# Kernel optimization log

Measured on AMD Instinct MI355X. Metric: run time of the kernel, lower is better.

The kernel has to match this reference:

```python
import jax, jax.numpy as jnp
import numpy as np
from jax import lax

HEADS, DIM = 8, 8
T = HEADS * DIM            # total_dim = 64
C_IN, C_OUT = 256, 256
B, H, W = 8, 128, 128
BN_EPS = 1e-5


def setup_inputs() -> dict:
    key = jax.random.key(0)
    ks = jax.random.split(key, 9)
    return {
        "x": jax.random.normal(ks[0], (B, C_IN, H, W), jnp.float32),
        "W_qkv": jax.random.normal(ks[1], (3 * T, C_IN), jnp.float32) * 0.05,
        "W_p": jax.random.normal(ks[2], (3 * HEADS, DIM, DIM), jnp.float32) * 0.1,
        "W_d": jax.random.normal(ks[3], (3 * T, 1, 3, 3), jnp.float32) * 0.1,
        "W_ffn": jax.random.normal(ks[4], (C_OUT, 2 * T), jnp.float32) * 0.1,
        "bn_gamma": jax.random.uniform(ks[5], (C_OUT,), jnp.float32, 0.5, 1.5),
        "bn_beta": jax.random.normal(ks[6], (C_OUT,), jnp.float32) * 0.1,
        "bn_mean": jax.random.normal(ks[7], (C_OUT,), jnp.float32) * 0.1,
        "bn_var": jax.random.uniform(ks[8], (C_OUT,), jnp.float32, 0.5, 1.5),
    }


def reference(x, W_qkv, W_p, W_d, W_ffn, bn_gamma, bn_beta, bn_mean, bn_var):
    b, _, h, w = x.shape
    # qkv: 1x1 conv, no bias -> (B, 3T, H, W)
    qkv = jnp.einsum('bchw,oc->bohw', x, W_qkv)
    # p_conv: grouped 1x1 conv, groups = 3*heads, group size = dim
    p = qkv.reshape(b, 3 * HEADS, DIM, h, w)
    p = jnp.einsum('bgihw,goi->bgohw', p, W_p).reshape(b, 3 * T, h, w)
    # d_conv: depthwise 3x3 conv, padding 1
    d = lax.conv_general_dilated(
        p, W_d, window_strides=(1, 1), padding='SAME',
        dimension_numbers=('NCHW', 'OIHW', 'NCHW'), feature_group_count=3 * T)
    # multi-scale concat -> (B, 6T, H, W) -> (B, 2*heads, 3*dim, HW) -> (B, 2*heads, HW, 3*dim)
    g = jnp.concatenate([qkv, d], axis=1)
    g = g.reshape(b, 2 * HEADS, 3 * DIM, h * w).transpose(0, 1, 3, 2)
    q = jax.nn.relu(g[..., :DIM])
    k = jax.nn.relu(g[..., DIM:2 * DIM])
    v = g[..., 2 * DIM:]
    # padding trick: append a column of ones to v for normalization
    v1 = jnp.concatenate([v, jnp.ones(v.shape[:-1] + (1,), v.dtype)], axis=-1)
    kv = jnp.einsum('bgnd,bgne->bgde', k, v1)     # (B, 2h, dim, dim+1)
    o = jnp.einsum('bgnd,bgde->bgne', q, kv)      # (B, 2h, HW, dim+1)
    o = o[..., :DIM] / (o[..., DIM:] + 1e-15)
    o = o.transpose(0, 1, 3, 2).reshape(b, 2 * T, h, w)
    # ffn: 1x1 conv + BatchNorm (eval mode, running stats)
    y = jnp.einsum('bchw,oc->bohw', o, W_ffn)
    scale = bn_gamma / jnp.sqrt(bn_var + BN_EPS)
    return y * scale[:, None, None] + (bn_beta - bn_mean * scale)[:, None, None]
```

## Files before the change

kernel.cpp:

```cpp
#include <hip/hip_runtime.h>

#define NB    8
#define NCIN  256
#define NH    128
#define NW    128
#define NHW   16384
#define NQKV  192
#define NCOUT 256

#define K1_BK  16
#define K1_LDB 132
#define K1_LDA 64

__global__ __launch_bounds__(256) void k1_qkv(
    const float* __restrict__ x, const float* __restrict__ Wq,
    float* __restrict__ qkv)
{
  __shared__ float Bs[2][K1_BK][K1_LDB];
  __shared__ float As[2][K1_BK][K1_LDA];

  const int tid = threadIdx.x;
  const int b   = blockIdx.x >> 7;
  const int n0  = (blockIdx.x & 127) << 7;
  const int m0  = blockIdx.y << 6;

  const int bk = tid >> 4;
  const int bn = (tid & 15) << 3;
  const int am = tid >> 2;
  const int ak = (tid & 3) << 2;
  const float* bP = x + (size_t)b * NCIN * NHW + (size_t)bk * NHW + n0 + bn;
  const float* aP = Wq + ((size_t)(m0 + am) << 8) + ak;

  const int tx = tid & 31;
  const int ty = tid >> 5;

  float4 rb0, rb1, ra;
  rb0 = *(const float4*)(bP);
  rb1 = *(const float4*)(bP + 4);
  ra  = *(const float4*)(aP);

  *(float4*)&Bs[0][bk][bn]     = rb0;
  *(float4*)&Bs[0][bk][bn + 4] = rb1;
  As[0][ak + 0][am] = ra.x;
  As[0][ak + 1][am] = ra.y;
  As[0][ak + 2][am] = ra.z;
  As[0][ak + 3][am] = ra.w;
  __syncthreads();

  float acc[8][4];
#pragma unroll
  for (int i = 0; i < 8; ++i)
#pragma unroll
    for (int j = 0; j < 4; ++j) acc[i][j] = 0.f;

  int cur = 0;
  for (int t = 0; t < 16; ++t) {
    if (t < 15) {
      const float* bq = bP + (size_t)(t + 1) * K1_BK * NHW;
      rb0 = *(const float4*)(bq);
      rb1 = *(const float4*)(bq + 4);
      ra  = *(const float4*)(aP + (t + 1) * K1_BK);
    }

#pragma unroll
    for (int kk = 0; kk < K1_BK; ++kk) {
      const float4 a0 = *(const float4*)&As[cur][kk][ty * 4];
      const float4 a1 = *(const float4*)&As[cur][kk][32 + ty * 4];
      const float4 bv = *(const float4*)&Bs[cur][kk][tx * 4];
      const float a[8]  = {a0.x, a0.y, a0.z, a0.w, a1.x, a1.y, a1.z, a1.w};
      const float bb[4] = {bv.x, bv.y, bv.z, bv.w};
#pragma unroll
      for (int i = 0; i < 8; ++i)
#pragma unroll
        for (int j = 0; j < 4; ++j) acc[i][j] = fmaf(a[i], bb[j], acc[i][j]);
    }

    if (t < 15) {
      const int nxt = cur ^ 1;
      *(float4*)&Bs[nxt][bk][bn]     = rb0;
      *(float4*)&Bs[nxt][bk][bn + 4] = rb1;
      As[nxt][ak + 0][am] = ra.x;
      As[nxt][ak + 1][am] = ra.y;
      As[nxt][ak + 2][am] = ra.z;
      As[nxt][ak + 3][am] = ra.w;
      __syncthreads();
      cur = nxt;
    }
  }

  float* outB = qkv + (size_t)b * NQKV * NHW + n0 + tx * 4;
#pragma unroll
  for (int i = 0; i < 8; ++i) {
    const int m = m0 + ((i < 4) ? (ty * 4 + i) : (32 + ty * 4 + (i - 4)));
    float4 v = {acc[i][0], acc[i][1], acc[i][2], acc[i][3]};
    *(float4*)(outB + (size_t)m * NHW) = v;
  }
}

__global__ __launch_bounds__(256, 4) void k2_qkv_kv(
    const float* __restrict__ qkv, float* __restrict__ kvb)
{
  __shared__ float red[4 * 72];
  const int tid = threadIdx.x;
  const int gg  = blockIdx.y;
  const int P0  = blockIdx.x * 2048;
  const int b   = P0 >> 14;
  const int n0  = P0 & (NHW - 1);

  const float* base = qkv + ((size_t)b * NQKV + gg * 24) * NHW + n0 + tid;

  float acc[72];
#pragma unroll
  for (int i = 0; i < 72; i++) acc[i] = 0.f;

  for (int it = 0; it < 8; it++) {
    const int off = it * 256;
    float kk[8], vv[8];
#pragma unroll
    for (int j = 0; j < 8; j++) kk[j] = fmaxf(base[(size_t)(8 + j) * NHW + off], 0.f);
#pragma unroll
    for (int j = 0; j < 8; j++) vv[j] = base[(size_t)(16 + j) * NHW + off];
#pragma unroll
    for (int d = 0; d < 8; d++) {
#pragma unroll
      for (int e = 0; e < 8; e++) acc[d * 9 + e] = fmaf(kk[d], vv[e], acc[d * 9 + e]);
      acc[d * 9 + 8] += kk[d];
    }
  }

  const int wave = tid >> 6, lane = tid & 63;
#pragma unroll
  for (int i = 0; i < 72; i++) {
    float v = acc[i];
    v += __shfl_down(v, 32);
    v += __shfl_down(v, 16);
    v += __shfl_down(v, 8);
    v += __shfl_down(v, 4);
    v += __shfl_down(v, 2);
    v += __shfl_down(v, 1);
    if (lane == 0) red[wave * 72 + i] = v;
  }
  __syncthreads();
  if (tid < 72) {
    float s = red[tid] + red[72 + tid] + red[144 + tid] + red[216 + tid];
    atomicAdd(&kvb[((size_t)b * 16 + gg) * 72 + tid], s);
  }
}

#define HALO_W 34
#define HALO_H 18
#define NPOS   (HALO_W * HALO_H)

__global__ __launch_bounds__(256, 2) void k2_dw(
    const float* __restrict__ qkv, const float* __restrict__ Wp,
    const float* __restrict__ Wd, float* __restrict__ dq,
    float* __restrict__ kvb)
{
  __shared__ float pbuf[24 * NPOS];
  __shared__ float red[4 * 72];

  const int tid  = threadIdx.x;
  const int gg8  = blockIdx.y;
  const int bt   = blockIdx.x;
  const int b    = bt >> 5;
  const int tile = bt & 31;
  const int ty0  = (tile >> 2) * 16;
  const int tx0  = (tile & 3) * 32;

  const float* src = qkv + ((size_t)b * NQKV + gg8 * 24) * NHW;

  for (int idx = tid; idx < 24 * NPOS; idx += 256) {
    const int c = idx / NPOS, pos = idx % NPOS;
    const int hy = pos / HALO_W, hx = pos % HALO_W;
    const int y = ty0 + hy - 1, xx = tx0 + hx - 1;
    float v = 0.f;
    if (y >= 0 && y < NH && xx >= 0 && xx < NW) v = src[(size_t)c * NHW + y * NW + xx];
    pbuf[idx] = v;
  }
  __syncthreads();

  for (int t = tid; t < 3 * NPOS; t += 256) {
    const int gloc = t / NPOS, pos = t % NPOS;
    float qv[8];
#pragma unroll
    for (int i = 0; i < 8; i++) qv[i] = pbuf[(gloc * 8 + i) * NPOS + pos];
    const float* wp = Wp + (size_t)(gg8 * 3 + gloc) * 64;
#pragma unroll
    for (int o = 0; o < 8; o++) {
      float s = 0.f;
#pragma unroll
      for (int i = 0; i < 8; i++) s = fmaf(wp[o * 8 + i], qv[i], s);
      pbuf[(gloc * 8 + o) * NPOS + pos] = s;
    }
  }
  __syncthreads();

  float acc[72];
#pragma unroll
  for (int i = 0; i < 72; i++) acc[i] = 0.f;

  const float* wdb = Wd + (size_t)gg8 * 24 * 9;

  for (int pp = tid; pp < 512; pp += 256) {
    const int ty = pp >> 5, tx = pp & 31;
    const int n  = (ty0 + ty) * NW + (tx0 + tx);
    float kk[8], vv[8];
#pragma unroll
    for (int cc = 0; cc < 24; cc++) {
      const float* pb = pbuf + cc * NPOS + ty * HALO_W + tx;
      const float* w  = wdb + cc * 9;
      float s = 0.f;
      s = fmaf(w[0], pb[0], s);
      s = fmaf(w[1], pb[1], s);
      s = fmaf(w[2], pb[2], s);
      s = fmaf(w[3], pb[HALO_W + 0], s);
      s = fmaf(w[4], pb[HALO_W + 1], s);
      s = fmaf(w[5], pb[HALO_W + 2], s);
      s = fmaf(w[6], pb[2 * HALO_W + 0], s);
      s = fmaf(w[7], pb[2 * HALO_W + 1], s);
      s = fmaf(w[8], pb[2 * HALO_W + 2], s);
      if (cc < 8) {
        dq[((size_t)b * 64 + gg8 * 8 + cc) * NHW + n] = fmaxf(s, 0.f);
      } else if (cc < 16) {
        kk[cc - 8] = fmaxf(s, 0.f);
      } else {
        vv[cc - 16] = s;
      }
    }
#pragma unroll
    for (int d = 0; d < 8; d++) {
#pragma unroll
      for (int e = 0; e < 8; e++) acc[d * 9 + e] = fmaf(kk[d], vv[e], acc[d * 9 + e]);
      acc[d * 9 + 8] += kk[d];
    }
  }

  const int wave = tid >> 6, lane = tid & 63;
#pragma unroll
  for (int i = 0; i < 72; i++) {
    float v = acc[i];
    v += __shfl_down(v, 32);
    v += __shfl_down(v, 16);
    v += __shfl_down(v, 8);
    v += __shfl_down(v, 4);
    v += __shfl_down(v, 2);
    v += __shfl_down(v, 1);
    if (lane == 0) red[wave * 72 + i] = v;
  }
  __syncthreads();
  if (tid < 72) {
    float s = red[tid] + red[72 + tid] + red[144 + tid] + red[216 + tid];
    atomicAdd(&kvb[((size_t)b * 16 + (8 + gg8)) * 72 + tid], s);
  }
}

__global__ __launch_bounds__(256) void k3_attn_ffn(
    const float* __restrict__ qkv, const float* __restrict__ dq,
    const float* __restrict__ kvb, const float* __restrict__ Wf,
    const float* __restrict__ gamma, const float* __restrict__ beta,
    const float* __restrict__ mean, const float* __restrict__ var,
    float* __restrict__ out)
{
  __shared__ float wS[64 * 128];
  __shared__ float oS[2][8][256];

  const int tid = threadIdx.x;
  const int b   = blockIdx.x >> 6;
  const int n0  = (blockIdx.x & 63) << 8;
  const int m0  = blockIdx.y << 6;
  const int tx  = tid & 63;
  const int ty  = tid >> 6;

  {
    const float* wsrc = Wf + (size_t)m0 * 128;
#pragma unroll
    for (int i = 0; i < 8; ++i) {
      const int off = i * 1024 + tid * 4;
      *(float4*)&wS[off] = *(const float4*)&wsrc[off];
    }
  }

  float acc[16][4];
#pragma unroll
  for (int m = 0; m < 16; ++m)
#pragma unroll
    for (int p = 0; p < 4; ++p) acc[m][p] = 0.f;

  const float* kvB = kvb + (size_t)b * 16 * 72;

  for (int g = 0; g < 16; ++g) {
    const float* qp = (g < 8)
        ? qkv + ((size_t)b * NQKV + g * 24) * NHW + n0 + tid
        : dq  + ((size_t)b * 64 + (g - 8) * 8) * NHW + n0 + tid;
    float qv[8];
#pragma unroll
    for (int j = 0; j < 8; ++j) {
      const float v = qp[(size_t)j * NHW];
      qv[j] = (g < 8) ? fmaxf(v, 0.f) : v;
    }
    const float* kvg = kvB + g * 72;
    float num[9];
#pragma unroll
    for (int e = 0; e < 9; ++e) {
      float s = 0.f;
#pragma unroll
      for (int d = 0; d < 8; ++d) s = fmaf(qv[d], kvg[d * 9 + e], s);
      num[e] = s;
    }
    const float r = __builtin_amdgcn_rcpf(num[8] + 1e-15f);
    const int buf = g & 1;
#pragma unroll
    for (int e = 0; e < 8; ++e) oS[buf][e][tid] = num[e] * r;

    __syncthreads();

    float ov[4][8];
#pragma unroll
    for (int p = 0; p < 4; ++p)
#pragma unroll
      for (int e = 0; e < 8; ++e) ov[p][e] = oS[buf][e][tx + p * 64];

    const float* wrow = &wS[(ty * 16) * 128 + g * 8];
#pragma unroll
    for (int m = 0; m < 16; ++m) {
      const float4 w0 = *(const float4*)&wrow[m * 128];
      const float4 w1 = *(const float4*)&wrow[m * 128 + 4];
      const float w8[8] = {w0.x, w0.y, w0.z, w0.w, w1.x, w1.y, w1.z, w1.w};
#pragma unroll
      for (int p = 0; p < 4; ++p)
#pragma unroll
        for (int e = 0; e < 8; ++e)
          acc[m][p] = fmaf(ov[p][e], w8[e], acc[m][p]);
    }
  }

#pragma unroll
  for (int m = 0; m < 16; ++m) {
    const int oc = m0 + ty * 16 + m;
    const float sc = gamma[oc] * __builtin_amdgcn_rsqf(var[oc] + 1e-5f);
    const float bi = fmaf(-mean[oc], sc, beta[oc]);
    float* op = out + ((size_t)b * NCOUT + oc) * NHW + n0 + tx;
#pragma unroll
    for (int p = 0; p < 4; ++p) op[p * 64] = fmaf(acc[m][p], sc, bi);
  }
}

extern "C" void kernel_launch(void* const* d_in, const int* in_sizes, int n_in,
                              void* d_out, int out_size, void* d_ws, size_t ws_size,
                              hipStream_t stream) {
  const float* x     = (const float*)d_in[0];
  const float* Wq    = (const float*)d_in[1];
  const float* Wp    = (const float*)d_in[2];
  const float* Wd    = (const float*)d_in[3];
  const float* Wf    = (const float*)d_in[4];
  const float* gamma = (const float*)d_in[5];
  const float* beta  = (const float*)d_in[6];
  const float* mean  = (const float*)d_in[7];
  const float* var   = (const float*)d_in[8];
  float* out = (float*)d_out;

  char* ws = (char*)d_ws;
  float* qkv = (float*)ws;
  float* dq  = (float*)(ws + (size_t)100663296);
  float* kvb = (float*)(ws + (size_t)134217728);

  hipMemsetAsync(kvb, 0, (size_t)NB * 16 * 72 * sizeof(float), stream);

  k1_qkv<<<dim3(1024, 3), 256, 0, stream>>>(x, Wq, qkv);
  k2_qkv_kv<<<dim3(64, 8), 256, 0, stream>>>(qkv, kvb);
  k2_dw<<<dim3(256, 8), 256, 0, stream>>>(qkv, Wp, Wd, dq, kvb);
  k3_attn_ffn<<<dim3(512, 4), 256, 0, stream>>>(qkv, dq, kvb, Wf, gamma, beta,
                                                mean, var, out);
}
```

Baseline: 711.5 us.

## Fuse qkv KV reduction into depthwise kernel and vectorize two-pixel conv

Removes the separate k2_qkv_kv kernel and computes the raw-qkv K^T[V,1] reduction inside k2_dw from the halo tile already staged in shared memory, which avoids a second full read of the k/v channels from global memory. The halo load is restructured so each thread loads all 24 channels of one position, and the depthwise conv now computes two adjacent pixels per thread with float2 LDS reads and float2 stores. This saves one launch and about 64 MB of qkv reads, at the cost of an extra block reduction, an extra barrier and more register pressure in k2_dw.

```diff
diff --git a/kernel.cpp b/kernel.cpp
--- a/kernel.cpp
+++ b/kernel.cpp
@@ -97,56 +97,6 @@
   }
 }
 
-__global__ __launch_bounds__(256, 4) void k2_qkv_kv(
-    const float* __restrict__ qkv, float* __restrict__ kvb)
-{
-  __shared__ float red[4 * 72];
-  const int tid = threadIdx.x;
-  const int gg  = blockIdx.y;
-  const int P0  = blockIdx.x * 2048;
-  const int b   = P0 >> 14;
-  const int n0  = P0 & (NHW - 1);
-
-  const float* base = qkv + ((size_t)b * NQKV + gg * 24) * NHW + n0 + tid;
-
-  float acc[72];
-#pragma unroll
-  for (int i = 0; i < 72; i++) acc[i] = 0.f;
-
-  for (int it = 0; it < 8; it++) {
-    const int off = it * 256;
-    float kk[8], vv[8];
-#pragma unroll
-    for (int j = 0; j < 8; j++) kk[j] = fmaxf(base[(size_t)(8 + j) * NHW + off], 0.f);
-#pragma unroll
-    for (int j = 0; j < 8; j++) vv[j] = base[(size_t)(16 + j) * NHW + off];
-#pragma unroll
-    for (int d = 0; d < 8; d++) {
-#pragma unroll
-      for (int e = 0; e < 8; e++) acc[d * 9 + e] = fmaf(kk[d], vv[e], acc[d * 9 + e]);
-      acc[d * 9 + 8] += kk[d];
-    }
-  }
-
-  const int wave = tid >> 6, lane = tid & 63;
-#pragma unroll
-  for (int i = 0; i < 72; i++) {
-    float v = acc[i];
-    v += __shfl_down(v, 32);
-    v += __shfl_down(v, 16);
-    v += __shfl_down(v, 8);
-    v += __shfl_down(v, 4);
-    v += __shfl_down(v, 2);
-    v += __shfl_down(v, 1);
-    if (lane == 0) red[wave * 72 + i] = v;
-  }
-  __syncthreads();
-  if (tid < 72) {
-    float s = red[tid] + red[72 + tid] + red[144 + tid] + red[216 + tid];
-    atomicAdd(&kvb[((size_t)b * 16 + gg) * 72 + tid], s);
-  }
-}
-
 #define HALO_W 34
 #define HALO_H 18
 #define NPOS   (HALO_W * HALO_H)
@@ -169,15 +119,68 @@
 
   const float* src = qkv + ((size_t)b * NQKV + gg8 * 24) * NHW;
 
-  for (int idx = tid; idx < 24 * NPOS; idx += 256) {
-    const int c = idx / NPOS, pos = idx % NPOS;
-    const int hy = pos / HALO_W, hx = pos % HALO_W;
-    const int y = ty0 + hy - 1, xx = tx0 + hx - 1;
-    float v = 0.f;
-    if (y >= 0 && y < NH && xx >= 0 && xx < NW) v = src[(size_t)c * NHW + y * NW + xx];
-    pbuf[idx] = v;
+#pragma unroll
+  for (int p = 0; p < 3; ++p) {
+    const int pos = tid + p * 256;
+    if (pos < NPOS) {
+      const int hy = pos / HALO_W;
+      const int hx = pos - hy * HALO_W;
+      const int y  = ty0 + hy - 1;
+      const int xx = tx0 + hx - 1;
+      float* dp = pbuf + pos;
+      if (y >= 0 && y < NH && xx >= 0 && xx < NW) {
+        const float* sp = src + y * NW + xx;
+#pragma unroll
+        for (int c = 0; c < 24; ++c) dp[c * NPOS] = sp[(size_t)c * NHW];
+      } else {
+#pragma unroll
+        for (int c = 0; c < 24; ++c) dp[c * NPOS] = 0.f;
+      }
+    }
   }
   __syncthreads();
+
+  const int wave = tid >> 6, lane = tid & 63;
+  const int py = tid >> 4;
+  const int px = (tid & 15) << 1;
+
+  {
+    const int pos = (py + 1) * HALO_W + (px + 1);
+    float k0[8], k1[8], v0[8], v1[8];
+#pragma unroll
+    for (int j = 0; j < 8; ++j) {
+      const float* kp = pbuf + (8 + j) * NPOS + pos;
+      k0[j] = fmaxf(kp[0], 0.f);
+      k1[j] = fmaxf(kp[1], 0.f);
+      const float* vp = pbuf + (16 + j) * NPOS + pos;
+      v0[j] = vp[0];
+      v1[j] = vp[1];
+    }
+    float a[72];
+#pragma unroll
+    for (int d = 0; d < 8; ++d) {
+#pragma unroll
+      for (int e = 0; e < 8; ++e)
+        a[d * 9 + e] = fmaf(k0[d], v0[e], k1[d] * v1[e]);
+      a[d * 9 + 8] = k0[d] + k1[d];
+    }
+#pragma unroll
+    for (int i = 0; i < 72; ++i) {
+      float v = a[i];
+      v += __shfl_down(v, 32);
+      v += __shfl_down(v, 16);
+      v += __shfl_down(v, 8);
+      v += __shfl_down(v, 4);
+      v += __shfl_down(v, 2);
+      v += __shfl_down(v, 1);
+      if (lane == 0) red[wave * 72 + i] = v;
+    }
+    __syncthreads();
+    if (tid < 72) {
+      float s = red[tid] + red[72 + tid] + red[144 + tid] + red[216 + tid];
+      atomicAdd(&kvb[((size_t)b * 16 + gg8) * 72 + tid], s);
+    }
+  }
 
   for (int t = tid; t < 3 * NPOS; t += 256) {
     const int gloc = t / NPOS, pos = t % NPOS;
@@ -195,47 +198,51 @@
   }
   __syncthreads();
 
+  const float* wdb = Wd + (size_t)gg8 * 24 * 9;
+  const int n = (ty0 + py) * NW + (tx0 + px);
+
+  float kk0[8], kk1[8], vv0[8], vv1[8];
+#pragma unroll
+  for (int cc = 0; cc < 24; ++cc) {
+    const float* pb = pbuf + cc * NPOS + py * HALO_W + px;
+    const float2 r0a = *(const float2*)(pb);
+    const float2 r0b = *(const float2*)(pb + 2);
+    const float2 r1a = *(const float2*)(pb + HALO_W);
+    const float2 r1b = *(const float2*)(pb + HALO_W + 2);
+    const float2 r2a = *(const float2*)(pb + 2 * HALO_W);
+    const float2 r2b = *(const float2*)(pb + 2 * HALO_W + 2);
+    const float* w = wdb + cc * 9;
+    float s0 = 0.f, s1 = 0.f;
+    s0 = fmaf(w[0], r0a.x, s0);  s1 = fmaf(w[0], r0a.y, s1);
+    s0 = fmaf(w[1], r0a.y, s0);  s1 = fmaf(w[1], r0b.x, s1);
+    s0 = fmaf(w[2], r0b.x, s0);  s1 = fmaf(w[2], r0b.y, s1);
+    s0 = fmaf(w[3], r1a.x, s0);  s1 = fmaf(w[3], r1a.y, s1);
+    s0 = fmaf(w[4], r1a.y, s0);  s1 = fmaf(w[4], r1b.x, s1);
+    s0 = fmaf(w[5], r1b.x, s0);  s1 = fmaf(w[5], r1b.y, s1);
+    s0 = fmaf(w[6], r2a.x, s0);  s1 = fmaf(w[6], r2a.y, s1);
+    s0 = fmaf(w[7], r2a.y, s0);  s1 = fmaf(w[7], r2b.x, s1);
+    s0 = fmaf(w[8], r2b.x, s0);  s1 = fmaf(w[8], r2b.y, s1);
+    if (cc < 8) {
+      float2 o = {fmaxf(s0, 0.f), fmaxf(s1, 0.f)};
+      *(float2*)&dq[((size_t)b * 64 + gg8 * 8 + cc) * NHW + n] = o;
+    } else if (cc < 16) {
+      kk0[cc - 8] = fmaxf(s0, 0.f);
+      kk1[cc - 8] = fmaxf(s1, 0.f);
+    } else {
+      vv0[cc - 16] = s0;
+      vv1[cc - 16] = s1;
+    }
+  }
+
   float acc[72];
 #pragma unroll
-  for (int i = 0; i < 72; i++) acc[i] = 0.f;
-
-  const float* wdb = Wd + (size_t)gg8 * 24 * 9;
-
-  for (int pp = tid; pp < 512; pp += 256) {
-    const int ty = pp >> 5, tx = pp & 31;
-    const int n  = (ty0 + ty) * NW + (tx0 + tx);
-    float kk[8], vv[8];
-#pragma unroll
-    for (int cc = 0; cc < 24; cc++) {
-      const float* pb = pbuf + cc * NPOS + ty * HALO_W + tx;
-      const float* w  = wdb + cc * 9;
-      float s = 0.f;
-      s = fmaf(w[0], pb[0], s);
-      s = fmaf(w[1], pb[1], s);
-      s = fmaf(w[2], pb[2], s);
-      s = fmaf(w[3], pb[HALO_W + 0], s);
-      s = fmaf(w[4], pb[HALO_W + 1], s);
-      s = fmaf(w[5], pb[HALO_W + 2], s);
-      s = fmaf(w[6], pb[2 * HALO_W + 0], s);
-      s = fmaf(w[7], pb[2 * HALO_W + 1], s);
-      s = fmaf(w[8], pb[2 * HALO_W + 2], s);
-      if (cc < 8) {
-        dq[((size_t)b * 64 + gg8 * 8 + cc) * NHW + n] = fmaxf(s, 0.f);
-      } else if (cc < 16) {
-        kk[cc - 8] = fmaxf(s, 0.f);
-      } else {
-        vv[cc - 16] = s;
-      }
-    }
-#pragma unroll
-    for (int d = 0; d < 8; d++) {
-#pragma unroll
-      for (int e = 0; e < 8; e++) acc[d * 9 + e] = fmaf(kk[d], vv[e], acc[d * 9 + e]);
-      acc[d * 9 + 8] += kk[d];
-    }
-  }
-
-  const int wave = tid >> 6, lane = tid & 63;
+  for (int d = 0; d < 8; ++d) {
+#pragma unroll
+    for (int e = 0; e < 8; ++e)
+      acc[d * 9 + e] = fmaf(kk0[d], vv0[e], kk1[d] * vv1[e]);
+    acc[d * 9 + 8] = kk0[d] + kk1[d];
+  }
+
 #pragma unroll
   for (int i = 0; i < 72; i++) {
     float v = acc[i];
@@ -367,7 +374,6 @@
   hipMemsetAsync(kvb, 0, (size_t)NB * 16 * 72 * sizeof(float), stream);
 
   k1_qkv<<<dim3(1024, 3), 256, 0, stream>>>(x, Wq, qkv);
-  k2_qkv_kv<<<dim3(64, 8), 256, 0, stream>>>(qkv, kvb);
   k2_dw<<<dim3(256, 8), 256, 0, stream>>>(qkv, Wp, Wd, dq, kvb);
   k3_attn_ffn<<<dim3(512, 4), 256, 0, stream>>>(qkv, dq, kvb, Wf, gamma, beta,
                                                 mean, var, out);
```

Measured after the change: 682.6 us. 1.04x faster.
